# Optimization experiments

Measured on AMD Instinct MI355X. Metric: run time of the kernel, lower is better.

Reference implementation:

```python
import jax, jax.numpy as jnp
import numpy as np

TEMP = 1.0

def setup_inputs() -> dict:
    key = jax.random.key(0)
    k1, k2, k3 = jax.random.split(key, 3)
    B, C, H, W = 8, 256, 64, 64
    h = jax.random.normal(k1, (B, C, H, W), dtype=jnp.float32)
    xs = jax.random.normal(k2, (B, C, H, W), dtype=jnp.float32)
    ys = jax.random.normal(k3, (B, C, H, W), dtype=jnp.float32)
    return {"h": h, "xs": xs, "ys": ys}

def reference(h, xs, ys):
    B, C, H, W = h.shape
    Bs, Cs, Hs, Ws = xs.shape
    hf = h.reshape(B, C, H * W)            # [B, C, N]   N = H*W
    xf = xs.reshape(Bs, Cs, Hs * Ws)       # [B, C, M]   M = Hs*Ws
    yf = ys.reshape(ys.shape[0], ys.shape[1], -1)  # [B, C, M]
    # attention[b, n, m] = sum_c h[b,c,n] * xs[b,c,m]
    attn = jnp.einsum('bcn,bcm->bnm', hf, xf)
    attn = jax.nn.softmax(attn / TEMP, axis=2)  # softmax over support positions m
    # xxs[b, c, n] = sum_m ys[b,c,m] * attn[b,n,m]
    xxs = jnp.einsum('bcm,bnm->bcn', yf, attn)
    return xxs.reshape(B, C, H, W)
```

## Files before the change

### kernel.cpp

```cpp
#include <hip/hip_runtime.h>
#include <stdint.h>

#define B_ 8
#define C_ 256
#define N_ 4096
#define M_ 4096
#define NT 128
#define MT 64
#define L2E 1.44269504f

typedef _Float16 f16x8 __attribute__((ext_vector_type(8)));
typedef _Float16 f16x4 __attribute__((ext_vector_type(4)));
typedef _Float16 f16x2 __attribute__((ext_vector_type(2)));
typedef float f32x16 __attribute__((ext_vector_type(16)));
typedef unsigned int u32x4 __attribute__((ext_vector_type(4)));

__device__ __forceinline__ void async16(const _Float16* g, _Float16* l) {
    __builtin_amdgcn_global_load_lds(
        (const __attribute__((address_space(1))) void*)g,
        (__attribute__((address_space(3))) void*)l, 16, 0, 0);
}

__device__ __forceinline__ void plswap(unsigned &a, unsigned &b) {
    auto r = __builtin_amdgcn_permlane32_swap(a, b, false, false);
    a = r[0];
    b = r[1];
}

__global__ __launch_bounds__(256) void kPre(const float* __restrict__ xs,
                                            const float* __restrict__ ys,
                                            _Float16* __restrict__ kt,
                                            _Float16* __restrict__ vb) {
    int bx = blockIdx.x;
    int t = threadIdx.x;
    if (bx < 2048) {
        __shared__ float tile[64][65];
        int b = bx >> 8, rem = bx & 255;
        int c0 = (rem >> 6) * 64, m0 = (rem & 63) * 64;
        int cl = t >> 4, m4 = (t & 15) * 4;
#pragma unroll
        for (int i = 0; i < 4; i++) {
            int c = c0 + cl + i * 16;
            const float4 v = *(const float4*)(xs + ((size_t)(b * C_ + c) * M_) + m0 + m4);
            tile[m4 + 0][cl + i * 16] = v.x;
            tile[m4 + 1][cl + i * 16] = v.y;
            tile[m4 + 2][cl + i * 16] = v.z;
            tile[m4 + 3][cl + i * 16] = v.w;
        }
        __syncthreads();
        int ml = t >> 4, c4 = (t & 15) * 4;
#pragma unroll
        for (int i = 0; i < 4; i++) {
            int m = m0 + ml + i * 16;
            f16x4 o;
            o[0] = (_Float16)tile[ml + i * 16][c4 + 0];
            o[1] = (_Float16)tile[ml + i * 16][c4 + 1];
            o[2] = (_Float16)tile[ml + i * 16][c4 + 2];
            o[3] = (_Float16)tile[ml + i * 16][c4 + 3];
            *(f16x4*)(kt + ((size_t)(b * M_ + m) * C_) + c0 + c4) = o;
        }
    } else {
        size_t i = ((size_t)(bx - 2048) * 256 + t) * 4;
        float4 v = *(const float4*)(ys + i);
        f16x4 o;
        o[0] = (_Float16)v.x; o[1] = (_Float16)v.y;
        o[2] = (_Float16)v.z; o[3] = (_Float16)v.w;
        *(f16x4*)(vb + i) = o;
    }
}

__global__ __launch_bounds__(512, 1) void kAttn(const float* __restrict__ h,
                                                const _Float16* __restrict__ kt,
                                                const _Float16* __restrict__ vb,
                                                float* __restrict__ out) {
    __shared__ _Float16 sK[2][MT * 256];

    const int t = threadIdx.x;
    const int w = t >> 6, lane = t & 63, hh = lane >> 5, l31 = lane & 31;
    const int b = blockIdx.x & 7;
    const int n0 = (blockIdx.x >> 3) * NT;
    const int ns = w & 3, ch = w >> 2;

    const _Float16* srcKb = kt + (size_t)b * M_ * C_;
    const _Float16* srcVb = vb + (size_t)b * C_ * M_;

#pragma unroll
    for (int j = 0; j < 4; j++) {
        int row = w * 8 + j * 2 + hh;
        int logi = l31 ^ (row & 31);
        async16(srcKb + (size_t)row * C_ + logi * 8, &sK[0][(w * 8 + j * 2) * 256]);
    }

    f16x8 qf[16];
    {
        const float* hq = h + (size_t)b * C_ * N_ + n0 + ns * 32 + l31;
#pragma unroll
        for (int ks = 0; ks < 16; ks++) {
            f16x8 q;
#pragma unroll
            for (int i = 0; i < 8; i++)
                q[i] = (_Float16)hq[(size_t)(ks * 16 + hh * 8 + i) * N_];
            qf[ks] = q;
        }
    }

    f32x16 o[4];
#pragma unroll
    for (int cq = 0; cq < 4; cq++)
#pragma unroll
        for (int r = 0; r < 16; r++) o[cq][r] = 0.f;

    float mst = -3.0e38f, lp = 0.f;

    const size_t vr0 = (size_t)(ch * 128 + l31) * M_;
    const size_t vr1 = (size_t)(ch * 128 + 32 + l31) * M_;
    const size_t vr2 = (size_t)(ch * 128 + 64 + l31) * M_;
    const size_t vr3 = (size_t)(ch * 128 + 96 + l31) * M_;

    for (int it = 0; it < M_ / MT; it++) {
        const int cur = it & 1, nxt = cur ^ 1;
        const int m0i = it * MT;
        asm volatile("s_waitcnt vmcnt(0) lgkmcnt(0)" ::: "memory");
        __builtin_amdgcn_s_barrier();

        f16x8 vA0[4], vA1[4];
#pragma unroll
        for (int ks = 0; ks < 4; ks++) {
            vA0[ks] = *(const f16x8*)(srcVb + vr0 + m0i + ks * 16 + hh * 8);
            vA1[ks] = *(const f16x8*)(srcVb + vr1 + m0i + ks * 16 + hh * 8);
        }
        __builtin_amdgcn_sched_barrier(0);

        if (it + 1 < M_ / MT) {
            const _Float16* srcK = srcKb + (size_t)(m0i + MT) * C_;
#pragma unroll
            for (int j = 0; j < 4; j++) {
                int row = w * 8 + j * 2 + hh;
                int logi = l31 ^ (row & 31);
                async16(srcK + (size_t)row * C_ + logi * 8, &sK[nxt][(w * 8 + j * 2) * 256]);
            }
        }

        f32x16 sm0, sm1;
#pragma unroll
        for (int r = 0; r < 16; r++) { sm0[r] = 0.f; sm1[r] = 0.f; }
        __builtin_amdgcn_s_setprio(1);
#pragma unroll
        for (int ks = 0; ks < 16; ks++) {
            f16x8 bk0 = *(const f16x8*)(&sK[cur][(l31) * 256 + (((ks * 2 + hh) ^ l31) << 3)]);
            sm0 = __builtin_amdgcn_mfma_f32_32x32x16_f16(bk0, qf[ks], sm0, 0, 0, 0);
            f16x8 bk1 = *(const f16x8*)(&sK[cur][(32 + l31) * 256 + (((ks * 2 + hh) ^ l31) << 3)]);
            sm1 = __builtin_amdgcn_mfma_f32_32x32x16_f16(bk1, qf[ks], sm1, 0, 0, 0);
        }
        __builtin_amdgcn_s_setprio(0);

        float tm[8];
#pragma unroll
        for (int j = 0; j < 8; j++)
            tm[j] = fmaxf(fmaxf(sm0[j], sm0[j + 8]), fmaxf(sm1[j], sm1[j + 8]));
#pragma unroll
        for (int j = 0; j < 4; j++) tm[j] = fmaxf(tm[j], tm[j + 4]);
        float rowmax = fmaxf(fmaxf(tm[0], tm[1]), fmaxf(tm[2], tm[3]));
        rowmax = fmaxf(rowmax, __shfl_xor(rowmax, 32, 64));
        float al = 1.0f;
        if (rowmax > mst) { al = exp2f((mst - rowmax) * L2E); mst = rowmax; }
        const float mb = mst * L2E;
#pragma unroll
        for (int r = 0; r < 16; r++) {
            sm0[r] = exp2f(sm0[r] * L2E - mb);
            sm1[r] = exp2f(sm1[r] * L2E - mb);
        }
        float tp[8];
#pragma unroll
        for (int j = 0; j < 8; j++)
            tp[j] = (sm0[j] + sm0[j + 8]) + (sm1[j] + sm1[j + 8]);
#pragma unroll
        for (int j = 0; j < 4; j++) tp[j] += tp[j + 4];
        float ps = (tp[0] + tp[1]) + (tp[2] + tp[3]);
        ps += __shfl_xor(ps, 32, 64);
        lp = lp * al + ps;

        if (al != 1.0f) {
#pragma unroll
            for (int cq = 0; cq < 4; cq++)
#pragma unroll
                for (int r = 0; r < 16; r++) o[cq][r] *= al;
        }

        f16x8 pfr0, pfr1, pfr2, pfr3;
        {
            unsigned pk[8];
#pragma unroll
            for (int j = 0; j < 8; j++) {
                f16x2 pr;
                pr[0] = (_Float16)sm0[2 * j];
                pr[1] = (_Float16)sm0[2 * j + 1];
                pk[j] = __builtin_bit_cast(unsigned, pr);
            }
            plswap(pk[0], pk[2]);
            plswap(pk[1], pk[3]);
            plswap(pk[4], pk[6]);
            plswap(pk[5], pk[7]);
            u32x4 t0, t1;
            t0[0] = pk[0]; t0[1] = pk[1]; t0[2] = pk[2]; t0[3] = pk[3];
            t1[0] = pk[4]; t1[1] = pk[5]; t1[2] = pk[6]; t1[3] = pk[7];
            pfr0 = __builtin_bit_cast(f16x8, t0);
            pfr1 = __builtin_bit_cast(f16x8, t1);
        }
        {
            unsigned pk[8];
#pragma unroll
            for (int j = 0; j < 8; j++) {
                f16x2 pr;
                pr[0] = (_Float16)sm1[2 * j];
                pr[1] = (_Float16)sm1[2 * j + 1];
                pk[j] = __builtin_bit_cast(unsigned, pr);
            }
            plswap(pk[0], pk[2]);
            plswap(pk[1], pk[3]);
            plswap(pk[4], pk[6]);
            plswap(pk[5], pk[7]);
            u32x4 t0, t1;
            t0[0] = pk[0]; t0[1] = pk[1]; t0[2] = pk[2]; t0[3] = pk[3];
            t1[0] = pk[4]; t1[1] = pk[5]; t1[2] = pk[6]; t1[3] = pk[7];
            pfr2 = __builtin_bit_cast(f16x8, t0);
            pfr3 = __builtin_bit_cast(f16x8, t1);
        }

        f16x8 vB2[4], vB3[4];
#pragma unroll
        for (int ks = 0; ks < 4; ks++) {
            vB2[ks] = *(const f16x8*)(srcVb + vr2 + m0i + ks * 16 + hh * 8);
            vB3[ks] = *(const f16x8*)(srcVb + vr3 + m0i + ks * 16 + hh * 8);
        }
        __builtin_amdgcn_sched_barrier(0);

        __builtin_amdgcn_s_setprio(1);
        o[0] = __builtin_amdgcn_mfma_f32_32x32x16_f16(vA0[0], pfr0, o[0], 0, 0, 0);
        o[1] = __builtin_amdgcn_mfma_f32_32x32x16_f16(vA1[0], pfr0, o[1], 0, 0, 0);
        o[0] = __builtin_amdgcn_mfma_f32_32x32x16_f16(vA0[1], pfr1, o[0], 0, 0, 0);
        o[1] = __builtin_amdgcn_mfma_f32_32x32x16_f16(vA1[1], pfr1, o[1], 0, 0, 0);
        o[0] = __builtin_amdgcn_mfma_f32_32x32x16_f16(vA0[2], pfr2, o[0], 0, 0, 0);
        o[1] = __builtin_amdgcn_mfma_f32_32x32x16_f16(vA1[2], pfr2, o[1], 0, 0, 0);
        o[0] = __builtin_amdgcn_mfma_f32_32x32x16_f16(vA0[3], pfr3, o[0], 0, 0, 0);
        o[1] = __builtin_amdgcn_mfma_f32_32x32x16_f16(vA1[3], pfr3, o[1], 0, 0, 0);
        o[2] = __builtin_amdgcn_mfma_f32_32x32x16_f16(vB2[0], pfr0, o[2], 0, 0, 0);
        o[3] = __builtin_amdgcn_mfma_f32_32x32x16_f16(vB3[0], pfr0, o[3], 0, 0, 0);
        o[2] = __builtin_amdgcn_mfma_f32_32x32x16_f16(vB2[1], pfr1, o[2], 0, 0, 0);
        o[3] = __builtin_amdgcn_mfma_f32_32x32x16_f16(vB3[1], pfr1, o[3], 0, 0, 0);
        o[2] = __builtin_amdgcn_mfma_f32_32x32x16_f16(vB2[2], pfr2, o[2], 0, 0, 0);
        o[3] = __builtin_amdgcn_mfma_f32_32x32x16_f16(vB3[2], pfr2, o[3], 0, 0, 0);
        o[2] = __builtin_amdgcn_mfma_f32_32x32x16_f16(vB2[3], pfr3, o[2], 0, 0, 0);
        o[3] = __builtin_amdgcn_mfma_f32_32x32x16_f16(vB3[3], pfr3, o[3], 0, 0, 0);
        __builtin_amdgcn_s_setprio(0);
    }

    const float linv = 1.0f / lp;
#pragma unroll
    for (int cq = 0; cq < 4; cq++)
#pragma unroll
        for (int r = 0; r < 16; r++) {
            int c = ch * 128 + cq * 32 + (r & 3) + 8 * (r >> 2) + 4 * hh;
            out[((size_t)(b * C_ + c)) * N_ + n0 + ns * 32 + l31] = o[cq][r] * linv;
        }
}

extern "C" void kernel_launch(void* const* d_in, const int* in_sizes, int n_in,
                              void* d_out, int out_size, void* d_ws, size_t ws_size,
                              hipStream_t stream) {
    const float* h  = (const float*)d_in[0];
    const float* xs = (const float*)d_in[1];
    const float* ys = (const float*)d_in[2];
    float* out = (float*)d_out;

    _Float16* kt  = (_Float16*)d_ws;
    _Float16* vbb = kt + (size_t)B_ * M_ * C_;

    kPre<<<dim3(2048 + 8192), 256, 0, stream>>>(xs, ys, kt, vbb);
    kAttn<<<dim3(B_ * (N_ / NT)), 512, 0, stream>>>(h, kt, vbb, out);
}
```

Measured before the change: 411.5 us.

## Drop LDS staging of K, read keys directly from global into MFMA operands

Removes the shared-memory double buffer for K tiles along with its per-iteration barrier and async global-to-LDS loads. Each wave now loads its K fragments straight from global memory, relying on L1/L2 for reuse. Blocks shrink to 256 threads with NT=64 and launch bounds allow two blocks per CU, so the grid doubles and there is more scheduling freedom without block-wide sync. The cost is more redundant global and cache traffic for K, since the waves sharing a key tile no longer read it from one LDS copy.

```diff
diff --git a/kernel.cpp b/kernel.cpp
--- a/kernel.cpp
+++ b/kernel.cpp
@@ -5,7 +5,7 @@
 #define C_ 256
 #define N_ 4096
 #define M_ 4096
-#define NT 128
+#define NT 64
 #define MT 64
 #define L2E 1.44269504f
 
@@ -14,12 +14,6 @@
 typedef _Float16 f16x2 __attribute__((ext_vector_type(2)));
 typedef float f32x16 __attribute__((ext_vector_type(16)));
 typedef unsigned int u32x4 __attribute__((ext_vector_type(4)));
-
-__device__ __forceinline__ void async16(const _Float16* g, _Float16* l) {
-    __builtin_amdgcn_global_load_lds(
-        (const __attribute__((address_space(1))) void*)g,
-        (__attribute__((address_space(3))) void*)l, 16, 0, 0);
-}
 
 __device__ __forceinline__ void plswap(unsigned &a, unsigned &b) {
     auto r = __builtin_amdgcn_permlane32_swap(a, b, false, false);
@@ -69,27 +63,18 @@
     }
 }
 
-__global__ __launch_bounds__(512, 1) void kAttn(const float* __restrict__ h,
+__global__ __launch_bounds__(256, 2) void kAttn(const float* __restrict__ h,
                                                 const _Float16* __restrict__ kt,
                                                 const _Float16* __restrict__ vb,
                                                 float* __restrict__ out) {
-    __shared__ _Float16 sK[2][MT * 256];
-
     const int t = threadIdx.x;
     const int w = t >> 6, lane = t & 63, hh = lane >> 5, l31 = lane & 31;
     const int b = blockIdx.x & 7;
     const int n0 = (blockIdx.x >> 3) * NT;
-    const int ns = w & 3, ch = w >> 2;
-
-    const _Float16* srcKb = kt + (size_t)b * M_ * C_;
-    const _Float16* srcVb = vb + (size_t)b * C_ * M_;
-
-#pragma unroll
-    for (int j = 0; j < 4; j++) {
-        int row = w * 8 + j * 2 + hh;
-        int logi = l31 ^ (row & 31);
-        async16(srcKb + (size_t)row * C_ + logi * 8, &sK[0][(w * 8 + j * 2) * 256]);
-    }
+    const int ns = w & 1, ch = w >> 1;
+
+    const _Float16* srcK = kt + (size_t)b * M_ * C_;
+    const _Float16* srcV = vb + (size_t)b * C_ * M_;
 
     f16x8 qf[16];
     {
@@ -112,33 +97,22 @@
 
     float mst = -3.0e38f, lp = 0.f;
 
-    const size_t vr0 = (size_t)(ch * 128 + l31) * M_;
-    const size_t vr1 = (size_t)(ch * 128 + 32 + l31) * M_;
-    const size_t vr2 = (size_t)(ch * 128 + 64 + l31) * M_;
-    const size_t vr3 = (size_t)(ch * 128 + 96 + l31) * M_;
+    const _Float16* kRow0 = srcK + (size_t)(l31) * C_ + hh * 8;
+    const _Float16* kRow1 = srcK + (size_t)(32 + l31) * C_ + hh * 8;
+    const _Float16* vRow0 = srcV + (size_t)(ch * 128 +  0 + l31) * M_ + hh * 8;
+    const _Float16* vRow1 = srcV + (size_t)(ch * 128 + 32 + l31) * M_ + hh * 8;
+    const _Float16* vRow2 = srcV + (size_t)(ch * 128 + 64 + l31) * M_ + hh * 8;
+    const _Float16* vRow3 = srcV + (size_t)(ch * 128 + 96 + l31) * M_ + hh * 8;
 
     for (int it = 0; it < M_ / MT; it++) {
-        const int cur = it & 1, nxt = cur ^ 1;
         const int m0i = it * MT;
-        asm volatile("s_waitcnt vmcnt(0) lgkmcnt(0)" ::: "memory");
-        __builtin_amdgcn_s_barrier();
+        const size_t kOff = (size_t)m0i * C_;
 
         f16x8 vA0[4], vA1[4];
 #pragma unroll
         for (int ks = 0; ks < 4; ks++) {
-            vA0[ks] = *(const f16x8*)(srcVb + vr0 + m0i + ks * 16 + hh * 8);
-            vA1[ks] = *(const f16x8*)(srcVb + vr1 + m0i + ks * 16 + hh * 8);
-        }
-        __builtin_amdgcn_sched_barrier(0);
-
-        if (it + 1 < M_ / MT) {
-            const _Float16* srcK = srcKb + (size_t)(m0i + MT) * C_;
-#pragma unroll
-            for (int j = 0; j < 4; j++) {
-                int row = w * 8 + j * 2 + hh;
-                int logi = l31 ^ (row & 31);
-                async16(srcK + (size_t)row * C_ + logi * 8, &sK[nxt][(w * 8 + j * 2) * 256]);
-            }
+            vA0[ks] = *(const f16x8*)(vRow0 + m0i + ks * 16);
+            vA1[ks] = *(const f16x8*)(vRow1 + m0i + ks * 16);
         }
 
         f32x16 sm0, sm1;
@@ -147,10 +121,10 @@
         __builtin_amdgcn_s_setprio(1);
 #pragma unroll
         for (int ks = 0; ks < 16; ks++) {
-            f16x8 bk0 = *(const f16x8*)(&sK[cur][(l31) * 256 + (((ks * 2 + hh) ^ l31) << 3)]);
-            sm0 = __builtin_amdgcn_mfma_f32_32x32x16_f16(bk0, qf[ks], sm0, 0, 0, 0);
-            f16x8 bk1 = *(const f16x8*)(&sK[cur][(32 + l31) * 256 + (((ks * 2 + hh) ^ l31) << 3)]);
-            sm1 = __builtin_amdgcn_mfma_f32_32x32x16_f16(bk1, qf[ks], sm1, 0, 0, 0);
+            f16x8 a0 = *(const f16x8*)(kRow0 + kOff + ks * 16);
+            sm0 = __builtin_amdgcn_mfma_f32_32x32x16_f16(a0, qf[ks], sm0, 0, 0, 0);
+            f16x8 a1 = *(const f16x8*)(kRow1 + kOff + ks * 16);
+            sm1 = __builtin_amdgcn_mfma_f32_32x32x16_f16(a1, qf[ks], sm1, 0, 0, 0);
         }
         __builtin_amdgcn_s_setprio(0);
 
@@ -230,10 +204,9 @@
         f16x8 vB2[4], vB3[4];
 #pragma unroll
         for (int ks = 0; ks < 4; ks++) {
-            vB2[ks] = *(const f16x8*)(srcVb + vr2 + m0i + ks * 16 + hh * 8);
-            vB3[ks] = *(const f16x8*)(srcVb + vr3 + m0i + ks * 16 + hh * 8);
-        }
-        __builtin_amdgcn_sched_barrier(0);
+            vB2[ks] = *(const f16x8*)(vRow2 + m0i + ks * 16);
+            vB3[ks] = *(const f16x8*)(vRow3 + m0i + ks * 16);
+        }
 
         __builtin_amdgcn_s_setprio(1);
         o[0] = __builtin_amdgcn_mfma_f32_32x32x16_f16(vA0[0], pfr0, o[0], 0, 0, 0);
@@ -277,5 +250,5 @@
     _Float16* vbb = kt + (size_t)B_ * M_ * C_;
 
     kPre<<<dim3(2048 + 8192), 256, 0, stream>>>(xs, ys, kt, vbb);
-    kAttn<<<dim3(B_ * (N_ / NT)), 512, 0, stream>>>(h, kt, vbb, out);
-}
+    kAttn<<<dim3(B_ * (N_ / NT)), 256, 0, stream>>>(h, kt, vbb, out);
+}
```

New measurement: 799.2 us. 94.2% more time.
